# Kernel tuning notes

Measured on AMD Instinct MI355X. Metric: run time of the kernel, lower is better.

The kernel has to match this reference:

```python
import jax, jax.numpy as jnp
import numpy as np

B, S, H, NH, KVH, HD = 8, 4096, 4096, 32, 8, 128
STEP = 2048
EPS = 1e-6


def _rotate_half(x):
    x1, x2 = x[..., : HD // 2], x[..., HD // 2 :]
    return jnp.concatenate([-x2, x1], axis=-1)


def _rmsnorm(x, w):
    xf = x.astype(jnp.float32)
    var = jnp.mean(xf * xf, axis=-1, keepdims=True)
    return w * (xf * jax.lax.rsqrt(var + EPS)).astype(x.dtype)


def setup_inputs() -> dict:
    key = jax.random.key(0)
    ks = jax.random.split(key, 10)
    wscale = 0.02
    hidden_states = jax.random.normal(ks[0], (B, 1, H), jnp.float32)
    # RoPE angles for position STEP
    inv_freq = 1.0 / (10000.0 ** (jnp.arange(0, HD, 2, dtype=jnp.float32) / HD))
    ang = STEP * inv_freq  # [HD/2]
    emb = jnp.concatenate([ang, ang])  # [HD]
    cos = jnp.broadcast_to(jnp.cos(emb), (B, 1, HD)).astype(jnp.float32)
    sin = jnp.broadcast_to(jnp.sin(emb), (B, 1, HD)).astype(jnp.float32)
    key_cache = jax.random.normal(ks[1], (B, KVH, S, HD), jnp.float32)
    value_cache = jax.random.normal(ks[2], (B, KVH, S, HD), jnp.float32)
    # additive causal mask: rows 0..STEP, cols 0..S-1; -1e9 where col > row
    rows = jnp.arange(STEP + 1)[:, None]
    cols = jnp.arange(S)[None, :]
    causal_mask = jnp.where(cols <= rows, 0.0, -1e9).astype(jnp.float32)[None, None]
    q_w = jax.random.normal(ks[3], (H, NH * HD), jnp.float32) * wscale
    k_w = jax.random.normal(ks[4], (H, KVH * HD), jnp.float32) * wscale
    v_w = jax.random.normal(ks[5], (H, KVH * HD), jnp.float32) * wscale
    o_w = jax.random.normal(ks[6], (NH * HD, H), jnp.float32) * wscale
    q_norm_w = jnp.ones((HD,), jnp.float32)
    k_norm_w = jnp.ones((HD,), jnp.float32)
    return {
        "hidden_states": hidden_states, "cos": cos, "sin": sin,
        "key_cache": key_cache, "value_cache": value_cache,
        "causal_mask": causal_mask, "q_w": q_w, "k_w": k_w, "v_w": v_w,
        "o_w": o_w, "q_norm_w": q_norm_w, "k_norm_w": k_norm_w,
        "step_idx": STEP,
    }


def reference(hidden_states, cos, sin, key_cache, value_cache, causal_mask,
              q_w, k_w, v_w, o_w, q_norm_w, k_norm_w, step_idx):
    G = NH // KVH
    scaling = HD ** -0.5
    bsz = hidden_states.shape[0]
    # projections + QK-RMSNorm; (B,1,nH,HD) -> (B,nH,1,HD)
    q = _rmsnorm((hidden_states @ q_w).reshape(bsz, 1, NH, HD), q_norm_w).transpose(0, 2, 1, 3)
    k = _rmsnorm((hidden_states @ k_w).reshape(bsz, 1, KVH, HD), k_norm_w).transpose(0, 2, 1, 3)
    v = (hidden_states @ v_w).reshape(bsz, 1, KVH, HD).transpose(0, 2, 1, 3)
    # RoPE (cos/sin broadcast over head axis)
    c = cos[:, None, :, :]  # (B,1,1,HD)
    s = sin[:, None, :, :]
    q = q * c + _rotate_half(q) * s
    k = k * c + _rotate_half(k) * s
    # single-step cache write
    key_cache = key_cache.at[:, :, step_idx : step_idx + 1].set(k)
    value_cache = value_cache.at[:, :, step_idx : step_idx + 1].set(v)
    # GQA attention without materializing repeat_kv (same math)
    qg = q.reshape(bsz, KVH, G, 1, HD)
    scores = jnp.einsum("bkgqd,bksd->bkgqs", qg, key_cache) * scaling  # (B,KVH,G,1,S)
    scores = scores.reshape(bsz, NH, 1, S) + causal_mask[:, :, step_idx : step_idx + 1, :]
    attn = jax.nn.softmax(scores.astype(jnp.float32), axis=-1).astype(q.dtype)
    out = jnp.einsum("bkgqs,bksd->bkgqd", attn.reshape(bsz, KVH, G, 1, S), value_cache)
    out = out.reshape(bsz, NH, 1, HD).transpose(0, 2, 1, 3).reshape(bsz, 1, NH * HD)
    return out @ o_w
```

## Files before the change

kernel.cpp:

```cpp
#include <hip/hip_runtime.h>
#include <math.h>

#define Bq 8
#define Sq 4096
#define Hq 4096
#define NHq 32
#define KVHq 8
#define HDq 128
#define QKV_N 6144
#define CHUNK 256
#define NCHUNK 16
#define ROWS 256

__global__ __launch_bounds__(256) void gemv_splitk(
    const float* __restrict__ x, const float* __restrict__ W,
    float* __restrict__ y, int K, int ldW, int ldY) {
  __shared__ float xs[Bq][ROWS];
  int tid = threadIdx.x;
  int r0 = blockIdx.y * ROWS;
  for (int i = tid; i < Bq * ROWS; i += 256) {
    int b = i >> 8, r = i & (ROWS - 1);
    xs[b][r] = x[b * K + r0 + r];
  }
  __syncthreads();
  int col = blockIdx.x * 256 + tid;
  float acc[Bq] = {0, 0, 0, 0, 0, 0, 0, 0};
  const float* wp = W + (size_t)r0 * ldW + col;
  for (int r = 0; r < ROWS; r += 8) {
    float w[8];
#pragma unroll
    for (int j = 0; j < 8; j++) w[j] = wp[(size_t)j * ldW];
    wp += (size_t)8 * ldW;
#pragma unroll
    for (int b = 0; b < Bq; b++) {
      float4 x0 = *(const float4*)&xs[b][r];
      float4 x1 = *(const float4*)&xs[b][r + 4];
      acc[b] = fmaf(x0.x, w[0], acc[b]);
      acc[b] = fmaf(x0.y, w[1], acc[b]);
      acc[b] = fmaf(x0.z, w[2], acc[b]);
      acc[b] = fmaf(x0.w, w[3], acc[b]);
      acc[b] = fmaf(x1.x, w[4], acc[b]);
      acc[b] = fmaf(x1.y, w[5], acc[b]);
      acc[b] = fmaf(x1.z, w[6], acc[b]);
      acc[b] = fmaf(x1.w, w[7], acc[b]);
    }
  }
#pragma unroll
  for (int b = 0; b < Bq; b++) atomicAdd(&y[b * ldY + col], acc[b]);
}

__global__ __launch_bounds__(256) void gemv_fused_qkv(
    const float* __restrict__ x, const float* __restrict__ qw,
    const float* __restrict__ kw, const float* __restrict__ vw,
    float* __restrict__ y) {
  __shared__ float xs[Bq][ROWS];
  int tid = threadIdx.x;
  int r0 = blockIdx.y * ROWS;
  for (int i = tid; i < Bq * ROWS; i += 256) {
    int b = i >> 8, r = i & (ROWS - 1);
    xs[b][r] = x[b * Hq + r0 + r];
  }
  __syncthreads();
  int col = blockIdx.x * 256 + tid;
  const float* W;
  int ldW, wcol;
  if (col < NHq * HDq) { W = qw; ldW = NHq * HDq; wcol = col; }
  else if (col < NHq * HDq + KVHq * HDq) { W = kw; ldW = KVHq * HDq; wcol = col - NHq * HDq; }
  else { W = vw; ldW = KVHq * HDq; wcol = col - (NHq + KVHq) * HDq; }
  float acc[Bq] = {0, 0, 0, 0, 0, 0, 0, 0};
  const float* wp = W + (size_t)r0 * ldW + wcol;
  for (int r = 0; r < ROWS; r += 8) {
    float w[8];
#pragma unroll
    for (int j = 0; j < 8; j++) w[j] = wp[(size_t)j * ldW];
    wp += (size_t)8 * ldW;
#pragma unroll
    for (int b = 0; b < Bq; b++) {
      float4 x0 = *(const float4*)&xs[b][r];
      float4 x1 = *(const float4*)&xs[b][r + 4];
      acc[b] = fmaf(x0.x, w[0], acc[b]);
      acc[b] = fmaf(x0.y, w[1], acc[b]);
      acc[b] = fmaf(x0.z, w[2], acc[b]);
      acc[b] = fmaf(x0.w, w[3], acc[b]);
      acc[b] = fmaf(x1.x, w[4], acc[b]);
      acc[b] = fmaf(x1.y, w[5], acc[b]);
      acc[b] = fmaf(x1.z, w[6], acc[b]);
      acc[b] = fmaf(x1.w, w[7], acc[b]);
    }
  }
#pragma unroll
  for (int b = 0; b < Bq; b++) atomicAdd(&y[b * QKV_N + col], acc[b]);
}

__global__ __launch_bounds__(256) void normrope(
    const float* __restrict__ qkv, const float* __restrict__ cosp,
    const float* __restrict__ sinp, const float* __restrict__ qnw,
    const float* __restrict__ knw, const int* __restrict__ step_ptr,
    float* __restrict__ kcache, float* __restrict__ vcache,
    float* __restrict__ qvec) {
  int tid = threadIdx.x;
  int lane = tid & 63, wid = tid >> 6;
  int vec = blockIdx.x * 4 + wid;
  int step = *step_ptr;
  if (vec < 256) {
    int b = vec >> 5, h = vec & 31;
    const float* src = qkv + b * QKV_N + h * HDq;
    float x0 = src[lane], x1 = src[lane + 64];
    float ss = fmaf(x0, x0, x1 * x1);
#pragma unroll
    for (int off = 32; off; off >>= 1) ss += __shfl_xor(ss, off, 64);
    float sc = rsqrtf(ss * (1.0f / HDq) + 1e-6f);
    float n0 = x0 * sc * qnw[lane], n1 = x1 * sc * qnw[lane + 64];
    float c0 = cosp[b * HDq + lane], c1 = cosp[b * HDq + lane + 64];
    float s0 = sinp[b * HDq + lane], s1 = sinp[b * HDq + lane + 64];
    float* dst = qvec + b * (NHq * HDq) + h * HDq;
    dst[lane] = fmaf(n0, c0, -n1 * s0);
    dst[lane + 64] = fmaf(n1, c1, n0 * s1);
  } else if (vec < 320) {
    int v = vec - 256;
    int b = v >> 3, kvh = v & 7;
    const float* src = qkv + b * QKV_N + NHq * HDq + kvh * HDq;
    float x0 = src[lane], x1 = src[lane + 64];
    float ss = fmaf(x0, x0, x1 * x1);
#pragma unroll
    for (int off = 32; off; off >>= 1) ss += __shfl_xor(ss, off, 64);
    float sc = rsqrtf(ss * (1.0f / HDq) + 1e-6f);
    float n0 = x0 * sc * knw[lane], n1 = x1 * sc * knw[lane + 64];
    float c0 = cosp[b * HDq + lane], c1 = cosp[b * HDq + lane + 64];
    float s0 = sinp[b * HDq + lane], s1 = sinp[b * HDq + lane + 64];
    float* dst = kcache + (((size_t)(b * KVHq + kvh)) * Sq + step) * HDq;
    dst[lane] = fmaf(n0, c0, -n1 * s0);
    dst[lane + 64] = fmaf(n1, c1, n0 * s1);
  } else {
    int v = vec - 320;
    int b = v >> 3, kvh = v & 7;
    const float* src = qkv + b * QKV_N + (NHq + KVHq) * HDq + kvh * HDq;
    float* dst = vcache + (((size_t)(b * KVHq + kvh)) * Sq + step) * HDq;
    dst[lane] = src[lane];
    dst[lane + 64] = src[lane + 64];
  }
}

__global__ __launch_bounds__(256) void attn_partial(
    const float* __restrict__ qvec, const float* __restrict__ kc,
    const float* __restrict__ vc, const int* __restrict__ step_ptr,
    float* __restrict__ pm, float* __restrict__ pl, float* __restrict__ po) {
  int c = blockIdx.x;
  int bk = blockIdx.y;
  int b = bk >> 3, kvh = bk & 7;
  int step = *step_ptr;
  int base = c * CHUNK;
  int pidx = (bk * NCHUNK + c) * 4;
  int tid = threadIdx.x;
  if (base > step) {
    if (tid < 4) { pm[pidx + tid] = -1e38f; pl[pidx + tid] = 0.0f; }
    return;
  }
  __shared__ float qs[4][HDq];
  __shared__ float red[4][4];
  __shared__ float pls[4][CHUNK];
  for (int i = tid; i < 4 * HDq; i += 256)
    qs[i >> 7][i & 127] = qvec[b * (NHq * HDq) + (kvh * 4 + (i >> 7)) * HDq + (i & 127)];
  __syncthreads();

  int s = base + tid;
  const float* krow = kc + (((size_t)bk) * Sq + s) * HDq;
  float sc[4] = {0, 0, 0, 0};
#pragma unroll 8
  for (int d = 0; d < HDq; d += 4) {
    float4 kk = *(const float4*)(krow + d);
#pragma unroll
    for (int g = 0; g < 4; g++) {
      float4 qq = *(const float4*)&qs[g][d];
      sc[g] += kk.x * qq.x + kk.y * qq.y + kk.z * qq.z + kk.w * qq.w;
    }
  }
  const float scaling = 0.08838834764831845f;
  bool valid = (s <= step);
#pragma unroll
  for (int g = 0; g < 4; g++) sc[g] = valid ? sc[g] * scaling : -1e30f;

  int lane = tid & 63, wid = tid >> 6;
#pragma unroll
  for (int g = 0; g < 4; g++) {
    float v = sc[g];
#pragma unroll
    for (int off = 32; off; off >>= 1) v = fmaxf(v, __shfl_xor(v, off, 64));
    if (lane == 0) red[g][wid] = v;
  }
  __syncthreads();
  float m[4];
#pragma unroll
  for (int g = 0; g < 4; g++)
    m[g] = fmaxf(fmaxf(red[g][0], red[g][1]), fmaxf(red[g][2], red[g][3]));
  __syncthreads();
#pragma unroll
  for (int g = 0; g < 4; g++) {
    float p = __expf(sc[g] - m[g]);
    pls[g][tid] = p;
    float v = p;
#pragma unroll
    for (int off = 32; off; off >>= 1) v += __shfl_xor(v, off, 64);
    if (lane == 0) red[g][wid] = v;
  }
  __syncthreads();
  if (tid < 4) {
    pm[pidx + tid] = m[tid];
    pl[pidx + tid] = red[tid][0] + red[tid][1] + red[tid][2] + red[tid][3];
  }
  int d = tid & 127, gp = tid >> 7;
  const float* vbase = vc + (((size_t)bk) * Sq + base) * HDq + d;
  float o0 = 0.0f, o1 = 0.0f;
#pragma unroll 4
  for (int ss = 0; ss < CHUNK; ss++) {
    float vv = vbase[(size_t)ss * HDq];
    o0 = fmaf(pls[gp][ss], vv, o0);
    o1 = fmaf(pls[gp + 2][ss], vv, o1);
  }
  po[(size_t)(pidx + gp) * HDq + d] = o0;
  po[(size_t)(pidx + gp + 2) * HDq + d] = o1;
}

__global__ __launch_bounds__(128) void attn_combine(
    const float* __restrict__ pm, const float* __restrict__ pl,
    const float* __restrict__ po, float* __restrict__ aout) {
  int bh = blockIdx.x;
  int b = bh >> 5, h = bh & 31;
  int kvh = h >> 2, g = h & 3;
  int d = threadIdx.x;
  int bk = b * KVHq + kvh;
  float mv[NCHUNK];
  float M = -1e38f;
#pragma unroll
  for (int c = 0; c < NCHUNK; c++) {
    mv[c] = pm[(bk * NCHUNK + c) * 4 + g];
    M = fmaxf(M, mv[c]);
  }
  float L = 0.0f, o = 0.0f;
#pragma unroll
  for (int c = 0; c < NCHUNK; c++) {
    if (mv[c] > -1e37f) {
      float w = __expf(mv[c] - M);
      L = fmaf(pl[(bk * NCHUNK + c) * 4 + g], w, L);
      o = fmaf(po[(size_t)((bk * NCHUNK + c) * 4 + g) * HDq + d], w, o);
    }
  }
  aout[b * (NHq * HDq) + h * HDq + d] = o / L;
}

extern "C" void kernel_launch(void* const* d_in, const int* in_sizes, int n_in,
                              void* d_out, int out_size, void* d_ws, size_t ws_size,
                              hipStream_t stream) {
  const float* hidden = (const float*)d_in[0];
  const float* cosp   = (const float*)d_in[1];
  const float* sinp   = (const float*)d_in[2];
  float* kcache       = (float*)d_in[3];
  float* vcache       = (float*)d_in[4];
  const float* q_w    = (const float*)d_in[6];
  const float* k_w    = (const float*)d_in[7];
  const float* v_w    = (const float*)d_in[8];
  const float* o_w    = (const float*)d_in[9];
  const float* qnw    = (const float*)d_in[10];
  const float* knw    = (const float*)d_in[11];
  const int* step_ptr = (const int*)d_in[12];
  float* out = (float*)d_out;
  float* ws = (float*)d_ws;

  float* qkv  = ws;
  float* qvec = ws + 49152;
  float* aout = ws + 81920;
  float* pm   = ws + 114688;
  float* pl   = ws + 118784;
  float* po   = ws + 122880;
  (void)in_sizes; (void)n_in; (void)ws_size;

  (void)hipMemsetAsync(qkv, 0, 49152 * sizeof(float), stream);
  (void)hipMemsetAsync(out, 0, (size_t)out_size * sizeof(float), stream);

  gemv_fused_qkv<<<dim3(QKV_N / 256, Hq / ROWS), 256, 0, stream>>>(hidden, q_w, k_w, v_w, qkv);

  normrope<<<96, 256, 0, stream>>>(qkv, cosp, sinp, qnw, knw, step_ptr, kcache, vcache, qvec);

  attn_partial<<<dim3(NCHUNK, Bq * KVHq), 256, 0, stream>>>(qvec, kcache, vcache, step_ptr, pm, pl, po);
  attn_combine<<<Bq * NHq, 128, 0, stream>>>(pm, pl, po, aout);

  gemv_splitk<<<dim3(16, Hq / ROWS), 256, 0, stream>>>(aout, o_w, out, NHq * HDq, 4096, 4096);
}
```

Before: 482.4 us.

## Halve GEMV split-K rows with deeper unroll and split PV accumulation across sequence halves

The split-K GEMV kernels now process 128 rows per block instead of 256, which doubles the grid and the number of atomics. Each thread now issues 16 weight loads per iteration instead of 8 to keep more memory requests in flight. In attention, each thread group now covers half of the chunk for all four query heads, instead of two heads over the full chunk. The two halves are combined through shared memory, so each V element is loaded once per thread and the P values are read as float4. The trade-off is twice the atomic traffic, more registers, and one extra barrier with shared-memory reduction.

```diff
diff --git a/kernel.cpp b/kernel.cpp
--- a/kernel.cpp
+++ b/kernel.cpp
@@ -10,7 +10,7 @@
 #define QKV_N 6144
 #define CHUNK 256
 #define NCHUNK 16
-#define ROWS 256
+#define ROWS 128
 
 __global__ __launch_bounds__(256) void gemv_splitk(
     const float* __restrict__ x, const float* __restrict__ W,
@@ -19,22 +19,24 @@
   int tid = threadIdx.x;
   int r0 = blockIdx.y * ROWS;
   for (int i = tid; i < Bq * ROWS; i += 256) {
-    int b = i >> 8, r = i & (ROWS - 1);
+    int b = i >> 7, r = i & (ROWS - 1);
     xs[b][r] = x[b * K + r0 + r];
   }
   __syncthreads();
   int col = blockIdx.x * 256 + tid;
   float acc[Bq] = {0, 0, 0, 0, 0, 0, 0, 0};
   const float* wp = W + (size_t)r0 * ldW + col;
-  for (int r = 0; r < ROWS; r += 8) {
-    float w[8];
-#pragma unroll
-    for (int j = 0; j < 8; j++) w[j] = wp[(size_t)j * ldW];
-    wp += (size_t)8 * ldW;
+  for (int r = 0; r < ROWS; r += 16) {
+    float w[16];
+#pragma unroll
+    for (int j = 0; j < 16; j++) w[j] = wp[(size_t)j * ldW];
+    wp += (size_t)16 * ldW;
 #pragma unroll
     for (int b = 0; b < Bq; b++) {
       float4 x0 = *(const float4*)&xs[b][r];
       float4 x1 = *(const float4*)&xs[b][r + 4];
+      float4 x2 = *(const float4*)&xs[b][r + 8];
+      float4 x3 = *(const float4*)&xs[b][r + 12];
       acc[b] = fmaf(x0.x, w[0], acc[b]);
       acc[b] = fmaf(x0.y, w[1], acc[b]);
       acc[b] = fmaf(x0.z, w[2], acc[b]);
@@ -43,6 +45,14 @@
       acc[b] = fmaf(x1.y, w[5], acc[b]);
       acc[b] = fmaf(x1.z, w[6], acc[b]);
       acc[b] = fmaf(x1.w, w[7], acc[b]);
+      acc[b] = fmaf(x2.x, w[8], acc[b]);
+      acc[b] = fmaf(x2.y, w[9], acc[b]);
+      acc[b] = fmaf(x2.z, w[10], acc[b]);
+      acc[b] = fmaf(x2.w, w[11], acc[b]);
+      acc[b] = fmaf(x3.x, w[12], acc[b]);
+      acc[b] = fmaf(x3.y, w[13], acc[b]);
+      acc[b] = fmaf(x3.z, w[14], acc[b]);
+      acc[b] = fmaf(x3.w, w[15], acc[b]);
     }
   }
 #pragma unroll
@@ -57,7 +67,7 @@
   int tid = threadIdx.x;
   int r0 = blockIdx.y * ROWS;
   for (int i = tid; i < Bq * ROWS; i += 256) {
-    int b = i >> 8, r = i & (ROWS - 1);
+    int b = i >> 7, r = i & (ROWS - 1);
     xs[b][r] = x[b * Hq + r0 + r];
   }
   __syncthreads();
@@ -69,15 +79,17 @@
   else { W = vw; ldW = KVHq * HDq; wcol = col - (NHq + KVHq) * HDq; }
   float acc[Bq] = {0, 0, 0, 0, 0, 0, 0, 0};
   const float* wp = W + (size_t)r0 * ldW + wcol;
-  for (int r = 0; r < ROWS; r += 8) {
-    float w[8];
-#pragma unroll
-    for (int j = 0; j < 8; j++) w[j] = wp[(size_t)j * ldW];
-    wp += (size_t)8 * ldW;
+  for (int r = 0; r < ROWS; r += 16) {
+    float w[16];
+#pragma unroll
+    for (int j = 0; j < 16; j++) w[j] = wp[(size_t)j * ldW];
+    wp += (size_t)16 * ldW;
 #pragma unroll
     for (int b = 0; b < Bq; b++) {
       float4 x0 = *(const float4*)&xs[b][r];
       float4 x1 = *(const float4*)&xs[b][r + 4];
+      float4 x2 = *(const float4*)&xs[b][r + 8];
+      float4 x3 = *(const float4*)&xs[b][r + 12];
       acc[b] = fmaf(x0.x, w[0], acc[b]);
       acc[b] = fmaf(x0.y, w[1], acc[b]);
       acc[b] = fmaf(x0.z, w[2], acc[b]);
@@ -86,6 +98,14 @@
       acc[b] = fmaf(x1.y, w[5], acc[b]);
       acc[b] = fmaf(x1.z, w[6], acc[b]);
       acc[b] = fmaf(x1.w, w[7], acc[b]);
+      acc[b] = fmaf(x2.x, w[8], acc[b]);
+      acc[b] = fmaf(x2.y, w[9], acc[b]);
+      acc[b] = fmaf(x2.z, w[10], acc[b]);
+      acc[b] = fmaf(x2.w, w[11], acc[b]);
+      acc[b] = fmaf(x3.x, w[12], acc[b]);
+      acc[b] = fmaf(x3.y, w[13], acc[b]);
+      acc[b] = fmaf(x3.z, w[14], acc[b]);
+      acc[b] = fmaf(x3.w, w[15], acc[b]);
     }
   }
 #pragma unroll
@@ -159,6 +179,7 @@
   __shared__ float qs[4][HDq];
   __shared__ float red[4][4];
   __shared__ float pls[4][CHUNK];
+  __shared__ float ored[2][4][HDq];
   for (int i = tid; i < 4 * HDq; i += 256)
     qs[i >> 7][i & 127] = qvec[b * (NHq * HDq) + (kvh * 4 + (i >> 7)) * HDq + (i & 127)];
   __syncthreads();
@@ -208,17 +229,32 @@
     pm[pidx + tid] = m[tid];
     pl[pidx + tid] = red[tid][0] + red[tid][1] + red[tid][2] + red[tid][3];
   }
-  int d = tid & 127, gp = tid >> 7;
-  const float* vbase = vc + (((size_t)bk) * Sq + base) * HDq + d;
-  float o0 = 0.0f, o1 = 0.0f;
+  int d = tid & 127, h = tid >> 7;
+  const float* vb = vc + (((size_t)bk) * Sq + base + h * (CHUNK / 2)) * HDq + d;
+  float o[4] = {0, 0, 0, 0};
 #pragma unroll 4
-  for (int ss = 0; ss < CHUNK; ss++) {
-    float vv = vbase[(size_t)ss * HDq];
-    o0 = fmaf(pls[gp][ss], vv, o0);
-    o1 = fmaf(pls[gp + 2][ss], vv, o1);
-  }
-  po[(size_t)(pidx + gp) * HDq + d] = o0;
-  po[(size_t)(pidx + gp + 2) * HDq + d] = o1;
+  for (int ss = 0; ss < CHUNK / 2; ss += 4) {
+    float vv0 = vb[(size_t)(ss + 0) * HDq];
+    float vv1 = vb[(size_t)(ss + 1) * HDq];
+    float vv2 = vb[(size_t)(ss + 2) * HDq];
+    float vv3 = vb[(size_t)(ss + 3) * HDq];
+#pragma unroll
+    for (int g = 0; g < 4; g++) {
+      float4 p = *(const float4*)&pls[g][h * (CHUNK / 2) + ss];
+      o[g] = fmaf(p.x, vv0, o[g]);
+      o[g] = fmaf(p.y, vv1, o[g]);
+      o[g] = fmaf(p.z, vv2, o[g]);
+      o[g] = fmaf(p.w, vv3, o[g]);
+    }
+  }
+#pragma unroll
+  for (int g = 0; g < 4; g++) ored[h][g][d] = o[g];
+  __syncthreads();
+  if (h == 0) {
+#pragma unroll
+    for (int g = 0; g < 4; g++)
+      po[(size_t)(pidx + g) * HDq + d] = ored[0][g][d] + ored[1][g][d];
+  }
 }
 
 __global__ __launch_bounds__(128) void attn_combine(
```

After: 428.0 us. 1.13x faster.
